# Performance work log

Hardware: AMD Instinct MI355X
Metric: run time of the kernel (lower is better)

Reference implementation:

```python
import jax, jax.numpy as jnp
import numpy as np

QUERY_DIM = 1024
CONTEXT_DIM = 1024
HEADS = 8
DIM_HEAD = 64
INNER = HEADS * DIM_HEAD  # 512
SCALE = DIM_HEAD ** -0.5


def setup_inputs() -> dict:
    key = jax.random.key(0)
    ks = jax.random.split(key, 7)
    B, N, M = 2, 2048, 2048
    x = jax.random.normal(ks[0], (B, N, QUERY_DIM), dtype=jnp.float32)
    context = jax.random.normal(ks[1], (B, M, CONTEXT_DIM), dtype=jnp.float32)
    # nn.Linear weights (stored as [out, in] in torch; we use [in, out] here)
    Wq = jax.random.normal(ks[2], (QUERY_DIM, INNER), dtype=jnp.float32) * (QUERY_DIM ** -0.5)
    Wk = jax.random.normal(ks[3], (CONTEXT_DIM, INNER), dtype=jnp.float32) * (CONTEXT_DIM ** -0.5)
    Wv = jax.random.normal(ks[4], (CONTEXT_DIM, INNER), dtype=jnp.float32) * (CONTEXT_DIM ** -0.5)
    Wo = jax.random.normal(ks[5], (INNER, QUERY_DIM), dtype=jnp.float32) * (INNER ** -0.5)
    bo = jax.random.normal(ks[6], (QUERY_DIM,), dtype=jnp.float32) * 0.01
    return {"x": x, "context": context, "Wq": Wq, "Wk": Wk, "Wv": Wv, "Wo": Wo, "bo": bo}


def reference(x, context, Wq, Wk, Wv, Wo, bo):
    B, N, _ = x.shape
    M = context.shape[1]
    # projections (no bias, matching nn.Linear(bias=False))
    q = (x @ Wq).reshape(B, N, HEADS, DIM_HEAD)          # b i h d
    k = (context @ Wk).reshape(B, M, HEADS, DIM_HEAD)    # b j h d
    v = (context @ Wv).reshape(B, M, HEADS, DIM_HEAD)    # b j h d
    # scores in fp32 (ATTN_PRECISION=='fp32' path)
    sim = jnp.einsum('bihd,bjhd->bhij', q.astype(jnp.float32), k.astype(jnp.float32)) * SCALE
    attn = jax.nn.softmax(sim, axis=-1).astype(v.dtype)  # b h i j
    out = jnp.einsum('bhij,bjhd->bihd', attn, v).reshape(B, N, INNER)
    return out @ Wo + bo  # dropout p=0.0 is identity
```

## Files before the change

### kernel.cpp

```cpp
#include <hip/hip_runtime.h>
#include <math.h>

typedef __bf16 bf16_t;
typedef __bf16 bf16x8 __attribute__((ext_vector_type(8)));
typedef __bf16 bf16x4 __attribute__((ext_vector_type(4)));
typedef float  f32x4  __attribute__((ext_vector_type(4)));

#define MFMA16(a, b, c) __builtin_amdgcn_mfma_f32_16x16x32_bf16((a), (b), (c), 0, 0, 0)

#define INNER   512
#define DHEAD   64
#define QSCALE  0.18033688f

__device__ __forceinline__ void g2l(const bf16_t* g, bf16_t* l) {
  __builtin_amdgcn_global_load_lds(
      (const __attribute__((address_space(1))) unsigned int*)g,
      (__attribute__((address_space(3))) unsigned int*)l, 16, 0, 0);
}

__global__ __launch_bounds__(256) void pre_k(const float* __restrict__ x,
                                             const float* __restrict__ ctx,
                                             const float* __restrict__ Wq,
                                             const float* __restrict__ Wk,
                                             const float* __restrict__ Wv,
                                             const float* __restrict__ Wo,
                                             bf16_t* __restrict__ xb,
                                             bf16_t* __restrict__ cb,
                                             bf16_t* __restrict__ WqT,
                                             bf16_t* __restrict__ WkT,
                                             bf16_t* __restrict__ WvT,
                                             bf16_t* __restrict__ WoT) {
  __shared__ float tile[64][65];
  int bx = blockIdx.x;
  if (bx < 8192) {
    const float* in = (bx >= 4096) ? ctx : x;
    bf16_t* out     = (bx >= 4096) ? cb  : xb;
    int i = (bx & 4095) * 256 + threadIdx.x;
    float4 f = ((const float4*)in)[i];
    bf16x4 v = { (bf16_t)f.x, (bf16_t)f.y, (bf16_t)f.z, (bf16_t)f.w };
    ((bf16x4*)out)[i] = v;
    return;
  }
  int t = bx - 8192;
  int z = t >> 7, bid = t & 127;
  const float* W; bf16_t* WT; int K, N;
  if (z == 0)      { W = Wq; WT = WqT; K = 1024; N = 512; }
  else if (z == 1) { W = Wk; WT = WkT; K = 1024; N = 512; }
  else if (z == 2) { W = Wv; WT = WvT; K = 1024; N = 512; }
  else             { W = Wo; WT = WoT; K = 512;  N = 1024; }
  int tK = K >> 6;
  int kt = bid % tK, nt = bid / tK;
  int k0 = kt << 6, n0 = nt << 6;
  for (int idx = threadIdx.x; idx < 4096; idx += 256) {
    int r = idx >> 6, c = idx & 63;
    tile[r][c] = W[(size_t)(k0 + r) * N + n0 + c];
  }
  __syncthreads();
  for (int idx = threadIdx.x; idx < 4096; idx += 256) {
    int r = idx >> 6, c = idx & 63;
    WT[(size_t)(n0 + r) * K + k0 + c] = (bf16_t)tile[c][r];
  }
}

__device__ __forceinline__ void gemm128(const bf16_t* __restrict__ A,
                                        const bf16_t* __restrict__ Bt,
                                        int K, int N, int row0, int n0,
                                        int mode, float scale,
                                        bf16_t* __restrict__ Cb,
                                        float* __restrict__ Cf,
                                        const float* __restrict__ bias) {
  __shared__ bf16_t As[128 * 32];
  __shared__ bf16_t Bs[128 * 32];
  const int tid = threadIdx.x;
  const int w = tid >> 6, lane = tid & 63, quad = lane >> 4, l16 = lane & 15;

  const int srow = lane >> 2;
  const int logc = (lane & 3) ^ ((lane >> 3) & 3);
  const bf16_t* gaw = A  + (size_t)(row0 + w * 32 + srow) * K + logc * 8;
  const bf16_t* gbw = Bt + (size_t)(n0   + w * 32 + srow) * K + logc * 8;
  bf16_t* lA = As + w * 1024;
  bf16_t* lB = Bs + w * 1024;

  f32x4 acc[4][4];
#pragma unroll
  for (int i = 0; i < 4; ++i)
#pragma unroll
    for (int j = 0; j < 4; ++j) acc[i][j] = f32x4{0.f, 0.f, 0.f, 0.f};

  const int mrow = (w & 1) << 6, ncol = (w >> 1) << 6;
  const int rphys = (quad ^ ((l16 >> 1) & 3)) << 3;
  const int KT = K >> 5;

  for (int kc = 0; kc < KT; ++kc) {
    __syncthreads();
    g2l(gaw + kc * 32,                   lA);
    g2l(gaw + (size_t)16 * K + kc * 32,  lA + 512);
    g2l(gbw + kc * 32,                   lB);
    g2l(gbw + (size_t)16 * K + kc * 32,  lB + 512);
    __syncthreads();
    bf16x8 af[4], bfr[4];
#pragma unroll
    for (int i = 0; i < 4; ++i)
      af[i] = *(const bf16x8*)&As[(mrow + i * 16 + l16) * 32 + rphys];
#pragma unroll
    for (int j = 0; j < 4; ++j)
      bfr[j] = *(const bf16x8*)&Bs[(ncol + j * 16 + l16) * 32 + rphys];
#pragma unroll
    for (int i = 0; i < 4; ++i)
#pragma unroll
      for (int j = 0; j < 4; ++j)
        acc[i][j] = MFMA16(af[i], bfr[j], acc[i][j]);
  }

#pragma unroll
  for (int i = 0; i < 4; ++i) {
    int row = row0 + mrow + i * 16 + quad * 4;
#pragma unroll
    for (int j = 0; j < 4; ++j) {
      int col = n0 + ncol + j * 16 + l16;
      if (mode == 2) {
        int bb = row >> 11, key = row & 2047;
        int hh = col >> 6,  d   = col & 63;
        bf16x4 v = { (bf16_t)acc[i][j][0], (bf16_t)acc[i][j][1],
                     (bf16_t)acc[i][j][2], (bf16_t)acc[i][j][3] };
        *(bf16x4*)&Cb[((size_t)((bb * 8 + hh) * 64 + d)) * 2048 + key] = v;
      } else {
#pragma unroll
        for (int r = 0; r < 4; ++r) {
          if (mode == 1) Cf[(size_t)(row + r) * N + col] = acc[i][j][r] + bias[col];
          else           Cb[(size_t)(row + r) * N + col] = (bf16_t)(acc[i][j][r] * scale);
        }
      }
    }
  }
}

__global__ __launch_bounds__(256, 2) void gemm_qkv_k(const bf16_t* __restrict__ xb,
                                                     const bf16_t* __restrict__ cb,
                                                     const bf16_t* __restrict__ WqT,
                                                     const bf16_t* __restrict__ WkT,
                                                     const bf16_t* __restrict__ WvT,
                                                     bf16_t* __restrict__ Qb,
                                                     bf16_t* __restrict__ Kb,
                                                     bf16_t* __restrict__ Vt) {
  int z = blockIdx.z;
  const bf16_t* A  = (z == 0) ? xb  : cb;
  const bf16_t* Bt = (z == 0) ? WqT : (z == 1) ? WkT : WvT;
  bf16_t* C        = (z == 0) ? Qb  : (z == 1) ? Kb  : Vt;
  int mode         = (z == 2) ? 2 : 0;
  float scale      = (z == 0) ? QSCALE : 1.0f;
  gemm128(A, Bt, 1024, 512, blockIdx.y * 128, blockIdx.x * 128, mode, scale,
          C, nullptr, nullptr);
}

__global__ __launch_bounds__(256, 2) void gemm_out_k(const bf16_t* __restrict__ AO,
                                                     const bf16_t* __restrict__ WoT,
                                                     const float* __restrict__ bo,
                                                     float* __restrict__ out) {
  gemm128(AO, WoT, 512, 1024, blockIdx.y * 128, blockIdx.x * 128, 1, 1.0f,
          nullptr, out, bo);
}

__global__ __launch_bounds__(256, 2) void attn_k(const bf16_t* __restrict__ Qb,
                                                 const bf16_t* __restrict__ Kb,
                                                 const bf16_t* __restrict__ Vt,
                                                 bf16_t* __restrict__ AO) {
  const int tid = threadIdx.x;
  const int w = tid >> 6, lane = tid & 63, quad = lane >> 4, l16 = lane & 15;
  const int qt = blockIdx.x;
  const int bh = blockIdx.y;
  const int b = bh >> 3, h = bh & 7;

  __shared__ bf16_t Ks[2 * 128 * 64];
  __shared__ bf16_t Vs[64 * 128];
  __shared__ bf16_t Ps[64 * 136];

  const int qrow = b * 2048 + qt * 64 + w * 16 + l16;
  const bf16_t* qptr = Qb + (size_t)qrow * INNER + h * DHEAD;
  bf16x8 bq[2];
  bq[0] = *(const bf16x8*)(qptr + quad * 8);
  bq[1] = *(const bf16x8*)(qptr + 32 + quad * 8);

  f32x4 o[4];
#pragma unroll
  for (int dt = 0; dt < 4; ++dt) o[dt] = f32x4{0.f, 0.f, 0.f, 0.f};
  float m_s = -__builtin_inff(), l_s = 0.f;

  const bf16_t* kbase  = Kb + ((size_t)b * 2048) * INNER + h * DHEAD;
  const bf16_t* vtbase = Vt + ((size_t)bh * 64) * 2048;

  const int krow = lane >> 3;
  const int kcol = ((lane & 7) ^ (lane >> 3)) << 3;
  const int vrow = lane >> 4;

#pragma unroll
  for (int p = 0; p < 4; ++p)
    g2l(kbase + (size_t)(w * 32 + p * 8 + krow) * INNER + kcol,
        &Ks[w * 2048 + p * 512]);

  for (int kt = 0; kt < 16; ++kt) {
    const int cur = (kt & 1) * 8192, nxt = ((kt + 1) & 1) * 8192;
    __syncthreads();
    if (kt < 16 - 1) {
#pragma unroll
      for (int p = 0; p < 4; ++p)
        g2l(kbase + (size_t)((kt + 1) * 128 + w * 32 + p * 8 + krow) * INNER + kcol,
            &Ks[nxt + w * 2048 + p * 512]);
    }
#pragma unroll
    for (int p = 0; p < 4; ++p) {
      int vlog = ((lane & 15) ^ ((p * 4 + vrow) & 15)) << 3;
      g2l(vtbase + (size_t)(w * 16 + p * 4 + vrow) * 2048 + kt * 128 + vlog,
          &Vs[w * 2048 + p * 512]);
    }

    f32x4 s[8];
#pragma unroll
    for (int jt = 0; jt < 8; ++jt) s[jt] = f32x4{0.f, 0.f, 0.f, 0.f};
#pragma unroll
    for (int jt = 0; jt < 8; ++jt) {
#pragma unroll
      for (int ks = 0; ks < 2; ++ks) {
        int phys = ((ks * 4 + quad) ^ (l16 & 7)) << 3;
        bf16x8 ak = *(const bf16x8*)&Ks[cur + (jt * 16 + l16) * 64 + phys];
        s[jt] = MFMA16(ak, bq[ks], s[jt]);
      }
    }

    float mx = -__builtin_inff();
#pragma unroll
    for (int jt = 0; jt < 8; ++jt) {
      float a = fmaxf(fmaxf(s[jt][0], s[jt][1]), fmaxf(s[jt][2], s[jt][3]));
      mx = fmaxf(mx, a);
    }
    mx = fmaxf(mx, __shfl_xor(mx, 16, 64));
    mx = fmaxf(mx, __shfl_xor(mx, 32, 64));
    float mnew = fmaxf(m_s, mx);
    float alpha = __builtin_amdgcn_exp2f(m_s - mnew);
    float rs = 0.f;
#pragma unroll
    for (int jt = 0; jt < 8; ++jt) {
#pragma unroll
      for (int r = 0; r < 4; ++r) {
        float p = __builtin_amdgcn_exp2f(s[jt][r] - mnew);
        s[jt][r] = p;
        rs += p;
      }
    }
    rs += __shfl_xor(rs, 16, 64);
    rs += __shfl_xor(rs, 32, 64);
    l_s = l_s * alpha + rs;
    m_s = mnew;
#pragma unroll
    for (int dt = 0; dt < 4; ++dt) o[dt] *= alpha;

#pragma unroll
    for (int jt = 0; jt < 8; ++jt) {
      bf16x4 pk = { (bf16_t)s[jt][0], (bf16_t)s[jt][1],
                    (bf16_t)s[jt][2], (bf16_t)s[jt][3] };
      *(bf16x4*)&Ps[(w * 16 + l16) * 136 + jt * 16 + quad * 4] = pk;
    }

    __syncthreads();

#pragma unroll
    for (int kc = 0; kc < 4; ++kc) {
      bf16x8 bp = *(const bf16x8*)&Ps[(w * 16 + l16) * 136 + kc * 32 + quad * 8];
#pragma unroll
      for (int dt = 0; dt < 4; ++dt) {
        int phys = ((kc * 4 + quad) ^ l16) << 3;
        bf16x8 av = *(const bf16x8*)&Vs[(dt * 16 + l16) * 128 + phys];
        o[dt] = MFMA16(av, bp, o[dt]);
      }
    }
  }

  float inv = 1.0f / l_s;
#pragma unroll
  for (int dt = 0; dt < 4; ++dt) {
    bf16x4 ov = { (bf16_t)(o[dt][0] * inv), (bf16_t)(o[dt][1] * inv),
                  (bf16_t)(o[dt][2] * inv), (bf16_t)(o[dt][3] * inv) };
    *(bf16x4*)&Ps[(w * 16 + l16) * 136 + dt * 16 + quad * 4] = ov;
  }
  __syncthreads();
  {
    int sr = tid >> 2, sc = (tid & 3) << 4;
    int4 r0 = *(const int4*)&Ps[sr * 136 + sc];
    int4 r1 = *(const int4*)&Ps[sr * 136 + sc + 8];
    bf16_t* aout = AO + ((size_t)(b * 2048 + qt * 64 + sr)) * INNER + h * DHEAD + sc;
    *(int4*)aout       = r0;
    *(int4*)(aout + 8) = r1;
  }
}

extern "C" void kernel_launch(void* const* d_in, const int* in_sizes, int n_in,
                              void* d_out, int out_size, void* d_ws, size_t ws_size,
                              hipStream_t stream) {
  const float* x   = (const float*)d_in[0];
  const float* ctx = (const float*)d_in[1];
  const float* Wq  = (const float*)d_in[2];
  const float* Wk  = (const float*)d_in[3];
  const float* Wv  = (const float*)d_in[4];
  const float* Wo  = (const float*)d_in[5];
  const float* bo  = (const float*)d_in[6];
  float* out = (float*)d_out;

  char* ws = (char*)d_ws;
  const size_t MB = 1048576;
  bf16_t* xb  = (bf16_t*)(ws + 0 * MB);
  bf16_t* cb  = (bf16_t*)(ws + 8 * MB);
  bf16_t* WqT = (bf16_t*)(ws + 16 * MB);
  bf16_t* WkT = (bf16_t*)(ws + 17 * MB);
  bf16_t* WvT = (bf16_t*)(ws + 18 * MB);
  bf16_t* WoT = (bf16_t*)(ws + 19 * MB);
  bf16_t* Qb  = (bf16_t*)(ws + 20 * MB);
  bf16_t* Kb  = (bf16_t*)(ws + 24 * MB);
  bf16_t* Vt  = (bf16_t*)(ws + 28 * MB);
  bf16_t* AO  = (bf16_t*)(ws + 32 * MB);

  pre_k<<<8704, 256, 0, stream>>>(x, ctx, Wq, Wk, Wv, Wo, xb, cb, WqT, WkT, WvT, WoT);
  gemm_qkv_k<<<dim3(4, 32, 3), 256, 0, stream>>>(xb, cb, WqT, WkT, WvT, Qb, Kb, Vt);
  attn_k<<<dim3(32, 16), 256, 0, stream>>>(Qb, Kb, Vt, AO);
  gemm_out_k<<<dim3(8, 32), 256, 0, stream>>>(AO, WoT, bo, out);
}
```

Baseline: 172.1 us.

## Fuse fp32-to-bf16 activation conversion into the QKV projection GEMM

Drops the separate conversion pass that wrote bf16 copies of x and context. The QKV GEMM now loads fp32 activations directly into registers, prefetches the next K-chunk, converts to bf16 and stores into swizzled LDS, while the weights still use the async global-to-LDS path. The goal is to remove a full write and re-read of 16 MB of activations. In exchange, the x tile is read twice as fp32 (double the bytes) across the 4 column blocks, and the A loads now go through registers instead of the async path. The output GEMM is inlined as its own kernel.

```diff
diff --git a/kernel.cpp b/kernel.cpp
--- a/kernel.cpp
+++ b/kernel.cpp
@@ -18,30 +18,16 @@
       (__attribute__((address_space(3))) unsigned int*)l, 16, 0, 0);
 }
 
-__global__ __launch_bounds__(256) void pre_k(const float* __restrict__ x,
-                                             const float* __restrict__ ctx,
-                                             const float* __restrict__ Wq,
+__global__ __launch_bounds__(256) void pre_k(const float* __restrict__ Wq,
                                              const float* __restrict__ Wk,
                                              const float* __restrict__ Wv,
                                              const float* __restrict__ Wo,
-                                             bf16_t* __restrict__ xb,
-                                             bf16_t* __restrict__ cb,
                                              bf16_t* __restrict__ WqT,
                                              bf16_t* __restrict__ WkT,
                                              bf16_t* __restrict__ WvT,
                                              bf16_t* __restrict__ WoT) {
   __shared__ float tile[64][65];
-  int bx = blockIdx.x;
-  if (bx < 8192) {
-    const float* in = (bx >= 4096) ? ctx : x;
-    bf16_t* out     = (bx >= 4096) ? cb  : xb;
-    int i = (bx & 4095) * 256 + threadIdx.x;
-    float4 f = ((const float4*)in)[i];
-    bf16x4 v = { (bf16_t)f.x, (bf16_t)f.y, (bf16_t)f.z, (bf16_t)f.w };
-    ((bf16x4*)out)[i] = v;
-    return;
-  }
-  int t = bx - 8192;
+  int t = blockIdx.x;
   int z = t >> 7, bid = t & 127;
   const float* W; bf16_t* WT; int K, N;
   if (z == 0)      { W = Wq; WT = WqT; K = 1024; N = 512; }
@@ -62,23 +48,34 @@
   }
 }
 
-__device__ __forceinline__ void gemm128(const bf16_t* __restrict__ A,
-                                        const bf16_t* __restrict__ Bt,
-                                        int K, int N, int row0, int n0,
-                                        int mode, float scale,
-                                        bf16_t* __restrict__ Cb,
-                                        float* __restrict__ Cf,
-                                        const float* __restrict__ bias) {
+__global__ __launch_bounds__(256, 2) void gemm_qkv_k(const float* __restrict__ x,
+                                                     const float* __restrict__ ctx,
+                                                     const bf16_t* __restrict__ WqT,
+                                                     const bf16_t* __restrict__ WkT,
+                                                     const bf16_t* __restrict__ WvT,
+                                                     bf16_t* __restrict__ Qb,
+                                                     bf16_t* __restrict__ Kb,
+                                                     bf16_t* __restrict__ Vt) {
+  const int z = blockIdx.z;
+  const float*  A  = (z == 0) ? x   : ctx;
+  const bf16_t* Bt = (z == 0) ? WqT : (z == 1) ? WkT : WvT;
+  bf16_t* C        = (z == 0) ? Qb  : (z == 1) ? Kb  : Vt;
+  const int mode   = (z == 2) ? 2 : 0;
+  const float scale = (z == 0) ? QSCALE : 1.0f;
+  const int K = 1024, K4 = 256, row0 = blockIdx.y * 128, n0 = blockIdx.x * 128;
+
   __shared__ bf16_t As[128 * 32];
   __shared__ bf16_t Bs[128 * 32];
   const int tid = threadIdx.x;
   const int w = tid >> 6, lane = tid & 63, quad = lane >> 4, l16 = lane & 15;
 
+  const int ar = tid >> 3;
+  const int ac = tid & 7;
+  const float4* agp = (const float4*)A + (size_t)(row0 + ar) * K4 + ac;
+  const int aoff0 = (ac & 1) * 4;
   const int srow = lane >> 2;
   const int logc = (lane & 3) ^ ((lane >> 3) & 3);
-  const bf16_t* gaw = A  + (size_t)(row0 + w * 32 + srow) * K + logc * 8;
-  const bf16_t* gbw = Bt + (size_t)(n0   + w * 32 + srow) * K + logc * 8;
-  bf16_t* lA = As + w * 1024;
+  const bf16_t* gbw = Bt + (size_t)(n0 + w * 32 + srow) * K + logc * 8;
   bf16_t* lB = Bs + w * 1024;
 
   f32x4 acc[4][4];
@@ -89,15 +86,29 @@
 
   const int mrow = (w & 1) << 6, ncol = (w >> 1) << 6;
   const int rphys = (quad ^ ((l16 >> 1) & 3)) << 3;
-  const int KT = K >> 5;
-
-  for (int kc = 0; kc < KT; ++kc) {
-    __syncthreads();
-    g2l(gaw + kc * 32,                   lA);
-    g2l(gaw + (size_t)16 * K + kc * 32,  lA + 512);
-    g2l(gbw + kc * 32,                   lB);
-    g2l(gbw + (size_t)16 * K + kc * 32,  lB + 512);
-    __syncthreads();
+
+  float4 apre[4];
+#pragma unroll
+  for (int i = 0; i < 4; ++i) apre[i] = agp[(size_t)(32 * i) * K4];
+
+  for (int kc = 0; kc < 32; ++kc) {
+    __syncthreads();
+#pragma unroll
+    for (int i = 0; i < 4; ++i) {
+      int r = ar + 32 * i;
+      int phys = (ac >> 1) ^ ((r >> 1) & 3);
+      bf16x4 v = { (bf16_t)apre[i].x, (bf16_t)apre[i].y,
+                   (bf16_t)apre[i].z, (bf16_t)apre[i].w };
+      *(bf16x4*)&As[r * 32 + phys * 8 + aoff0] = v;
+    }
+    g2l(gbw + kc * 32,                  lB);
+    g2l(gbw + (size_t)16 * K + kc * 32, lB + 512);
+    __syncthreads();
+    if (kc + 1 < 32) {
+#pragma unroll
+      for (int i = 0; i < 4; ++i)
+        apre[i] = agp[(size_t)(32 * i) * K4 + (kc + 1) * 8];
+    }
     bf16x8 af[4], bfr[4];
 #pragma unroll
     for (int i = 0; i < 4; ++i)
@@ -123,42 +134,73 @@
         int hh = col >> 6,  d   = col & 63;
         bf16x4 v = { (bf16_t)acc[i][j][0], (bf16_t)acc[i][j][1],
                      (bf16_t)acc[i][j][2], (bf16_t)acc[i][j][3] };
-        *(bf16x4*)&Cb[((size_t)((bb * 8 + hh) * 64 + d)) * 2048 + key] = v;
+        *(bf16x4*)&C[((size_t)((bb * 8 + hh) * 64 + d)) * 2048 + key] = v;
       } else {
 #pragma unroll
-        for (int r = 0; r < 4; ++r) {
-          if (mode == 1) Cf[(size_t)(row + r) * N + col] = acc[i][j][r] + bias[col];
-          else           Cb[(size_t)(row + r) * N + col] = (bf16_t)(acc[i][j][r] * scale);
-        }
+        for (int r = 0; r < 4; ++r)
+          C[(size_t)(row + r) * 512 + col] = (bf16_t)(acc[i][j][r] * scale);
       }
     }
   }
-}
-
-__global__ __launch_bounds__(256, 2) void gemm_qkv_k(const bf16_t* __restrict__ xb,
-                                                     const bf16_t* __restrict__ cb,
-                                                     const bf16_t* __restrict__ WqT,
-                                                     const bf16_t* __restrict__ WkT,
-                                                     const bf16_t* __restrict__ WvT,
-                                                     bf16_t* __restrict__ Qb,
-                                                     bf16_t* __restrict__ Kb,
-                                                     bf16_t* __restrict__ Vt) {
-  int z = blockIdx.z;
-  const bf16_t* A  = (z == 0) ? xb  : cb;
-  const bf16_t* Bt = (z == 0) ? WqT : (z == 1) ? WkT : WvT;
-  bf16_t* C        = (z == 0) ? Qb  : (z == 1) ? Kb  : Vt;
-  int mode         = (z == 2) ? 2 : 0;
-  float scale      = (z == 0) ? QSCALE : 1.0f;
-  gemm128(A, Bt, 1024, 512, blockIdx.y * 128, blockIdx.x * 128, mode, scale,
-          C, nullptr, nullptr);
 }
 
 __global__ __launch_bounds__(256, 2) void gemm_out_k(const bf16_t* __restrict__ AO,
                                                      const bf16_t* __restrict__ WoT,
                                                      const float* __restrict__ bo,
                                                      float* __restrict__ out) {
-  gemm128(AO, WoT, 512, 1024, blockIdx.y * 128, blockIdx.x * 128, 1, 1.0f,
-          nullptr, out, bo);
+  const int K = 512, N = 1024, row0 = blockIdx.y * 128, n0 = blockIdx.x * 128;
+  __shared__ bf16_t As[128 * 32];
+  __shared__ bf16_t Bs[128 * 32];
+  const int tid = threadIdx.x;
+  const int w = tid >> 6, lane = tid & 63, quad = lane >> 4, l16 = lane & 15;
+
+  const int srow = lane >> 2;
+  const int logc = (lane & 3) ^ ((lane >> 3) & 3);
+  const bf16_t* gaw = AO  + (size_t)(row0 + w * 32 + srow) * K + logc * 8;
+  const bf16_t* gbw = WoT + (size_t)(n0   + w * 32 + srow) * K + logc * 8;
+  bf16_t* lA = As + w * 1024;
+  bf16_t* lB = Bs + w * 1024;
+
+  f32x4 acc[4][4];
+#pragma unroll
+  for (int i = 0; i < 4; ++i)
+#pragma unroll
+    for (int j = 0; j < 4; ++j) acc[i][j] = f32x4{0.f, 0.f, 0.f, 0.f};
+
+  const int mrow = (w & 1) << 6, ncol = (w >> 1) << 6;
+  const int rphys = (quad ^ ((l16 >> 1) & 3)) << 3;
+
+  for (int kc = 0; kc < 16; ++kc) {
+    __syncthreads();
+    g2l(gaw + kc * 32,                  lA);
+    g2l(gaw + (size_t)16 * K + kc * 32, lA + 512);
+    g2l(gbw + kc * 32,                  lB);
+    g2l(gbw + (size_t)16 * K + kc * 32, lB + 512);
+    __syncthreads();
+    bf16x8 af[4], bfr[4];
+#pragma unroll
+    for (int i = 0; i < 4; ++i)
+      af[i] = *(const bf16x8*)&As[(mrow + i * 16 + l16) * 32 + rphys];
+#pragma unroll
+    for (int j = 0; j < 4; ++j)
+      bfr[j] = *(const bf16x8*)&Bs[(ncol + j * 16 + l16) * 32 + rphys];
+#pragma unroll
+    for (int i = 0; i < 4; ++i)
+#pragma unroll
+      for (int j = 0; j < 4; ++j)
+        acc[i][j] = MFMA16(af[i], bfr[j], acc[i][j]);
+  }
+#pragma unroll
+  for (int i = 0; i < 4; ++i) {
+    int row = row0 + mrow + i * 16 + quad * 4;
+#pragma unroll
+    for (int j = 0; j < 4; ++j) {
+      int col = n0 + ncol + j * 16 + l16;
+#pragma unroll
+      for (int r = 0; r < 4; ++r)
+        out[(size_t)(row + r) * N + col] = acc[i][j][r] + bo[col];
+    }
+  }
 }
 
 __global__ __launch_bounds__(256, 2) void attn_k(const bf16_t* __restrict__ Qb,
@@ -307,19 +349,17 @@
 
   char* ws = (char*)d_ws;
   const size_t MB = 1048576;
-  bf16_t* xb  = (bf16_t*)(ws + 0 * MB);
-  bf16_t* cb  = (bf16_t*)(ws + 8 * MB);
-  bf16_t* WqT = (bf16_t*)(ws + 16 * MB);
-  bf16_t* WkT = (bf16_t*)(ws + 17 * MB);
-  bf16_t* WvT = (bf16_t*)(ws + 18 * MB);
-  bf16_t* WoT = (bf16_t*)(ws + 19 * MB);
-  bf16_t* Qb  = (bf16_t*)(ws + 20 * MB);
-  bf16_t* Kb  = (bf16_t*)(ws + 24 * MB);
-  bf16_t* Vt  = (bf16_t*)(ws + 28 * MB);
-  bf16_t* AO  = (bf16_t*)(ws + 32 * MB);
-
-  pre_k<<<8704, 256, 0, stream>>>(x, ctx, Wq, Wk, Wv, Wo, xb, cb, WqT, WkT, WvT, WoT);
-  gemm_qkv_k<<<dim3(4, 32, 3), 256, 0, stream>>>(xb, cb, WqT, WkT, WvT, Qb, Kb, Vt);
+  bf16_t* WqT = (bf16_t*)(ws + 0 * MB);
+  bf16_t* WkT = (bf16_t*)(ws + 1 * MB);
+  bf16_t* WvT = (bf16_t*)(ws + 2 * MB);
+  bf16_t* WoT = (bf16_t*)(ws + 3 * MB);
+  bf16_t* Qb  = (bf16_t*)(ws + 4 * MB);
+  bf16_t* Kb  = (bf16_t*)(ws + 8 * MB);
+  bf16_t* Vt  = (bf16_t*)(ws + 12 * MB);
+  bf16_t* AO  = (bf16_t*)(ws + 16 * MB);
+
+  pre_k<<<512, 256, 0, stream>>>(Wq, Wk, Wv, Wo, WqT, WkT, WvT, WoT);
+  gemm_qkv_k<<<dim3(4, 32, 3), 256, 0, stream>>>(x, ctx, WqT, WkT, WvT, Qb, Kb, Vt);
   attn_k<<<dim3(32, 16), 256, 0, stream>>>(Qb, Kb, Vt, AO);
   gemm_out_k<<<dim3(8, 32), 256, 0, stream>>>(AO, WoT, bo, out);
 }
```

Measured after the change: 179.2 us. 4.1% more time.

## Double-buffer LDS tiles in projection GEMM with 64-wide K steps

Applied to the files above, without the earlier changes.

The shared 128x128 bf16 GEMM used for the projections now uses two LDS buffers and a K-step of 64 instead of 32. It prefetches the next K tile with global_load_lds while MFMAs run on the current one. The XOR swizzle is changed to an 8-way pattern to match the wider rows. This removes one barrier per step and hides global load latency, at the cost of four times the LDS per block, which may lower occupancy.

```diff
diff --git a/kernel.cpp b/kernel.cpp
--- a/kernel.cpp
+++ b/kernel.cpp
@@ -69,17 +69,17 @@
                                         bf16_t* __restrict__ Cb,
                                         float* __restrict__ Cf,
                                         const float* __restrict__ bias) {
-  __shared__ bf16_t As[128 * 32];
-  __shared__ bf16_t Bs[128 * 32];
+  __shared__ bf16_t As[2 * 128 * 64];
+  __shared__ bf16_t Bs[2 * 128 * 64];
   const int tid = threadIdx.x;
   const int w = tid >> 6, lane = tid & 63, quad = lane >> 4, l16 = lane & 15;
 
-  const int srow = lane >> 2;
-  const int logc = (lane & 3) ^ ((lane >> 3) & 3);
-  const bf16_t* gaw = A  + (size_t)(row0 + w * 32 + srow) * K + logc * 8;
-  const bf16_t* gbw = Bt + (size_t)(n0   + w * 32 + srow) * K + logc * 8;
-  bf16_t* lA = As + w * 1024;
-  bf16_t* lB = Bs + w * 1024;
+  const int sr8  = lane >> 3;
+  const int slog = ((lane & 7) ^ sr8) << 3;
+  const bf16_t* ga = A  + (size_t)(row0 + w * 32 + sr8) * K + slog;
+  const bf16_t* gb = Bt + (size_t)(n0   + w * 32 + sr8) * K + slog;
+  bf16_t* lA = As + w * 2048;
+  bf16_t* lB = Bs + w * 2048;
 
   f32x4 acc[4][4];
 #pragma unroll
@@ -88,28 +88,41 @@
     for (int j = 0; j < 4; ++j) acc[i][j] = f32x4{0.f, 0.f, 0.f, 0.f};
 
   const int mrow = (w & 1) << 6, ncol = (w >> 1) << 6;
-  const int rphys = (quad ^ ((l16 >> 1) & 3)) << 3;
-  const int KT = K >> 5;
+  const int KT = K >> 6;
+
+#pragma unroll
+  for (int p = 0; p < 4; ++p) {
+    g2l(ga + (size_t)(p * 8) * K, lA + p * 512);
+    g2l(gb + (size_t)(p * 8) * K, lB + p * 512);
+  }
 
   for (int kc = 0; kc < KT; ++kc) {
+    const int cur = (kc & 1) * 8192, nxt = ((kc + 1) & 1) * 8192;
     __syncthreads();
-    g2l(gaw + kc * 32,                   lA);
-    g2l(gaw + (size_t)16 * K + kc * 32,  lA + 512);
-    g2l(gbw + kc * 32,                   lB);
-    g2l(gbw + (size_t)16 * K + kc * 32,  lB + 512);
-    __syncthreads();
-    bf16x8 af[4], bfr[4];
-#pragma unroll
-    for (int i = 0; i < 4; ++i)
-      af[i] = *(const bf16x8*)&As[(mrow + i * 16 + l16) * 32 + rphys];
-#pragma unroll
-    for (int j = 0; j < 4; ++j)
-      bfr[j] = *(const bf16x8*)&Bs[(ncol + j * 16 + l16) * 32 + rphys];
-#pragma unroll
-    for (int i = 0; i < 4; ++i)
+    if (kc + 1 < KT) {
+      const int k0 = (kc + 1) * 64;
+#pragma unroll
+      for (int p = 0; p < 4; ++p) {
+        g2l(ga + (size_t)(p * 8) * K + k0, lA + nxt + p * 512);
+        g2l(gb + (size_t)(p * 8) * K + k0, lB + nxt + p * 512);
+      }
+    }
+#pragma unroll
+    for (int ks = 0; ks < 2; ++ks) {
+      const int phys = ((ks * 4 + quad) ^ (l16 & 7)) << 3;
+      bf16x8 af[4], bfr[4];
+#pragma unroll
+      for (int i = 0; i < 4; ++i)
+        af[i] = *(const bf16x8*)&As[cur + (mrow + i * 16 + l16) * 64 + phys];
 #pragma unroll
       for (int j = 0; j < 4; ++j)
-        acc[i][j] = MFMA16(af[i], bfr[j], acc[i][j]);
+        bfr[j] = *(const bf16x8*)&Bs[cur + (ncol + j * 16 + l16) * 64 + phys];
+#pragma unroll
+      for (int i = 0; i < 4; ++i)
+#pragma unroll
+        for (int j = 0; j < 4; ++j)
+          acc[i][j] = MFMA16(af[i], bfr[j], acc[i][j]);
+    }
   }
 
 #pragma unroll
```

Result: faster. 165.5 us (-3.8%).
